# Kernel tuning notes

Measured on AMD Instinct MI355X. Metric: run time of the kernel, lower is better.

The kernel has to match this reference:

```python
import jax, jax.numpy as jnp
import numpy as np

D, H, E, K, S = 1024, 2048, 8, 2, 1  # dim, expert hidden, n_experts, top_k, n_shared
B, L = 4, 2048


def setup_inputs() -> dict:
    key = jax.random.key(0)
    ks = jax.random.split(key, 9)
    std = 0.02
    return {
        "x": jax.random.normal(ks[0], (B, L, D), dtype=jnp.float32),
        "router_w": jax.random.normal(ks[1], (E, D), dtype=jnp.float32) * std,
        "experts_bias": jnp.zeros((E,), dtype=jnp.float32),  # aux-free LB bias buffer
        "w1": jax.random.normal(ks[2], (E, D, H), dtype=jnp.float32) * std,
        "w3": jax.random.normal(ks[3], (E, D, H), dtype=jnp.float32) * std,
        "w2": jax.random.normal(ks[4], (E, H, D), dtype=jnp.float32) * std,
        "sw1": jax.random.normal(ks[5], (S, D, H), dtype=jnp.float32) * std,
        "sw3": jax.random.normal(ks[6], (S, D, H), dtype=jnp.float32) * std,
        "sw2": jax.random.normal(ks[7], (S, H, D), dtype=jnp.float32) * std,
    }


def reference(x, router_w, experts_bias, w1, w3, w2, sw1, sw3, sw2):
    b, l, d = x.shape
    xf = x.reshape(-1, d)  # [T, D], T = b*l

    # shared experts (SwiGLU FFN), summed over S
    sg = jnp.einsum("td,sdh->tsh", xf, sw1)
    su = jnp.einsum("td,sdh->tsh", xf, sw3)
    shared_out = jnp.einsum("tsh,shd->td", jax.nn.silu(sg) * su, sw2)

    # router + aux-free load-balancing bias
    logits = xf @ router_w.T + experts_bias  # [T, E]
    rw, sel = jax.lax.top_k(logits, K)       # [T, K]
    rw = jax.nn.softmax(rw.astype(jnp.float32), axis=-1).astype(x.dtype)

    # combine weights scattered to [T, E]; equals torch one_hot dispatch+index_add
    cw = (jax.nn.one_hot(sel, E, dtype=x.dtype) * rw[..., None]).sum(axis=1)

    # all-expert SwiGLU, weighted-combined (identical math: unselected weight = 0)
    g = jnp.einsum("td,edh->teh", xf, w1)
    u = jnp.einsum("td,edh->teh", xf, w3)
    eo = jax.nn.silu(g) * u  # [T, E, H]
    moe_out = jnp.einsum("te,teh,ehd->td", cw, eo, w2)

    return (moe_out + shared_out).reshape(b, l, d)
```

## Files before the change

kernel.cpp:

```cpp
#include <hip/hip_runtime.h>
#include <stdint.h>

#define T_TOK 8192
#define DIMV  1024
#define HIDV  2048
#define NE    8
#define CAP   8192
#define ROUTED 16384
#define ASSIGN_TOT 24576
#define NCAT  4096

typedef __attribute__((ext_vector_type(8))) short          bf16x8;
typedef __attribute__((ext_vector_type(8))) unsigned short u16x8;
typedef __attribute__((ext_vector_type(4))) float          floatx4;

__device__ __forceinline__ unsigned short f2bf(float f) {
    union { float f; unsigned int i; } v; v.f = f;
    unsigned int i = v.i;
    return (unsigned short)((i + 0x7FFFu + ((i >> 16) & 1u)) >> 16);
}
__device__ __forceinline__ float bf2f(unsigned short u) {
    union { unsigned int i; float f; } v; v.i = ((unsigned int)u) << 16; return v.f;
}

__device__ __forceinline__ void gll16(const void* g, void* l) {
    __builtin_amdgcn_global_load_lds((const __attribute__((address_space(1))) void*)g,
                                     (__attribute__((address_space(3))) void*)l,
                                     16, 0, 0);
}

__global__ __launch_bounds__(256) void router_kernel(
    const float* __restrict__ x,
    const float* __restrict__ rwp,
    const float* __restrict__ biasp,
    unsigned short* __restrict__ xb,
    int* __restrict__ cnt, int* __restrict__ tlist,
    int* __restrict__ pos, float* __restrict__ pw)
{
    const int t    = blockIdx.x * 4 + (threadIdx.x >> 6);
    const int lane = threadIdx.x & 63;
    const float* xr = x + (size_t)t * DIMV + lane * 16;
    float xf[16];
#pragma unroll
    for (int q = 0; q < 4; q++) {
        float4 v = *(const float4*)(xr + q * 4);
        xf[q*4+0] = v.x; xf[q*4+1] = v.y; xf[q*4+2] = v.z; xf[q*4+3] = v.w;
    }
    {
        u16x8 o0, o1;
#pragma unroll
        for (int j = 0; j < 8; j++) { o0[j] = f2bf(xf[j]); o1[j] = f2bf(xf[8 + j]); }
        unsigned short* xo = xb + (size_t)t * DIMV + lane * 16;
        *(u16x8*)xo = o0;
        *(u16x8*)(xo + 8) = o1;
    }
    float acc[NE];
#pragma unroll
    for (int e = 0; e < NE; e++) {
        const float* wr = rwp + (size_t)e * DIMV + lane * 16;
        float s = 0.f;
#pragma unroll
        for (int q = 0; q < 4; q++) {
            float4 v = *(const float4*)(wr + q * 4);
            s += xf[q*4+0]*v.x + xf[q*4+1]*v.y + xf[q*4+2]*v.z + xf[q*4+3]*v.w;
        }
        acc[e] = s;
    }
#pragma unroll
    for (int e = 0; e < NE; e++)
#pragma unroll
        for (int off = 32; off; off >>= 1) acc[e] += __shfl_xor(acc[e], off, 64);

    if (lane == 0) {
        float lg[NE];
#pragma unroll
        for (int e = 0; e < NE; e++) lg[e] = acc[e] + biasp[e];
        int e0 = 0;
#pragma unroll
        for (int e = 1; e < NE; e++) if (lg[e] > lg[e0]) e0 = e;
        int e1 = (e0 == 0) ? 1 : 0;
#pragma unroll
        for (int e = 0; e < NE; e++) if (e != e0 && lg[e] > lg[e1]) e1 = e;
        float z  = __expf(lg[e1] - lg[e0]);
        float p0 = 1.f / (1.f + z);
        float p1 = z  / (1.f + z);
        int s0 = atomicAdd(cnt + e0, 1);
        tlist[e0 * CAP + s0] = t;
        int s1 = atomicAdd(cnt + e1, 1);
        tlist[e1 * CAP + s1] = t;
        pos[2 * t + 0] = e0 * CAP + s0;
        pos[2 * t + 1] = e1 * CAP + s1;
        pw[2 * t + 0] = p0;
        pw[2 * t + 1] = p1;
    }
}

template<int R, int C>
__device__ __forceinline__ void ctrans_body(
    const float* __restrict__ src, unsigned short* __restrict__ dstp,
    unsigned short (*tile)[66], int ileave, int ubit)
{
    const int c0 = blockIdx.x * 64, r0 = blockIdx.y * 64;
    const int tid = threadIdx.x;
    const int lr = tid >> 4;
    const int lc = (tid & 15) * 4;
#pragma unroll
    for (int i = 0; i < 4; i++) {
        int r = lr + 16 * i;
        float4 v = *(const float4*)(src + (size_t)(r0 + r) * C + (c0 + lc));
        ushort4 o; o.x = f2bf(v.x); o.y = f2bf(v.y); o.z = f2bf(v.z); o.w = f2bf(v.w);
        *(ushort4*)&tile[r][lc] = o;
    }
    __syncthreads();
    const int oc  = tid >> 3;
    const int orr = (tid & 7) * 8;
#pragma unroll
    for (int i = 0; i < 2; i++) {
        int c = oc + 32 * i;
        int h = c0 + c;
        int row = ileave ? (((h >> 4) << 5) + ubit * 16 + (h & 15)) : h;
        u16x8 tmp;
#pragma unroll
        for (int j = 0; j < 8; j++) tmp[j] = tile[orr + j][c];
        *(u16x8*)(dstp + (size_t)row * R + (r0 + orr)) = tmp;
    }
}

__global__ __launch_bounds__(256) void ctrans_all(
    const float* __restrict__ w1, const float* __restrict__ w3,
    const float* __restrict__ sw1, const float* __restrict__ sw3,
    const float* __restrict__ w2, const float* __restrict__ sw2,
    unsigned short* __restrict__ wcat, unsigned short* __restrict__ scat,
    unsigned short* __restrict__ w2t, unsigned short* __restrict__ sw2t)
{
    __shared__ unsigned short tile[64][66];
    const int z = blockIdx.z;
    if (z < 18) {
        if (blockIdx.y >= DIMV / 64) return;
        const float* src; unsigned short* dstp; int u;
        if (z < 8)        { src = w1 + (size_t)z * DIMV * HIDV;       dstp = wcat + (size_t)z * NCAT * DIMV;       u = 0; }
        else if (z < 16)  { src = w3 + (size_t)(z - 8) * DIMV * HIDV; dstp = wcat + (size_t)(z - 8) * NCAT * DIMV; u = 1; }
        else if (z == 16) { src = sw1; dstp = scat; u = 0; }
        else              { src = sw3; dstp = scat; u = 1; }
        ctrans_body<DIMV, HIDV>(src, dstp, tile, 1, u);
    } else {
        if (blockIdx.x >= DIMV / 64) return;
        const float* src; unsigned short* dstp;
        if (z < 26) { src = w2 + (size_t)(z - 18) * HIDV * DIMV; dstp = w2t + (size_t)(z - 18) * DIMV * HIDV; }
        else        { src = sw2; dstp = sw2t; }
        ctrans_body<HIDV, DIMV>(src, dstp, tile, 0, 0);
    }
}


__global__ __launch_bounds__(512, 2) void up_gemm8(
    const unsigned short* __restrict__ x,
    const unsigned short* __restrict__ wcat,
    const unsigned short* __restrict__ scat,
    const int* __restrict__ cnt, const int* __restrict__ tlist,
    unsigned short* __restrict__ hbuf)
{
    const int g = blockIdx.z;
    int n_rows, row_off = 0;
    const unsigned short* Bp;
    if (g < NE) {
        for (int e = 0; e < g; e++) row_off += cnt[e];
        n_rows = cnt[g];
        Bp = wcat + (size_t)g * NCAT * DIMV;
    } else { n_rows = T_TOK; row_off = ROUTED; Bp = scat; }
    const int m0 = blockIdx.y * 256;
    if (m0 >= n_rows) return;
    const int n0 = blockIdx.x * 256;

    extern __shared__ __align__(16) unsigned short smem[];
    unsigned short* As = smem;
    unsigned short* Bs = smem + 32768;

    const int tid  = threadIdx.x;
    const int lane = tid & 63;
    const int wave = tid >> 6;
    const int wm = wave >> 2, wn = wave & 3;
    const int m16 = lane & 15, quad = lane >> 4;

    const int sr = tid >> 2;
    const int sc = (((tid & 3) ^ ((sr >> 1) & 3)) << 3);

    int tA0, tA1;
    if (g < NE) {
        int ra = m0 + sr;       if (ra >= n_rows) ra = n_rows - 1;
        int rb = m0 + 128 + sr; if (rb >= n_rows) rb = n_rows - 1;
        tA0 = tlist[g * CAP + ra];
        tA1 = tlist[g * CAP + rb];
    } else { tA0 = m0 + sr; tA1 = m0 + 128 + sr; }
    const unsigned short* sA0 = x + (size_t)tA0 * DIMV + sc;
    const unsigned short* sA1 = x + (size_t)tA1 * DIMV + sc;
    const unsigned short* sB0 = Bp + (size_t)(n0 + sr) * DIMV + sc;
    const unsigned short* sB1 = Bp + (size_t)(n0 + 128 + sr) * DIMV + sc;

    unsigned short* dA = As + wave * 512;
    unsigned short* dB = Bs + wave * 512;

#define UPSA(t, kk) { unsigned short* d_ = dA + (((t) & 1) << 14) + ((kk) << 13); \
        gll16(sA0 + (t) * 64 + (kk) * 32, d_); gll16(sA1 + (t) * 64 + (kk) * 32, d_ + 4096); }
#define UPSB(t, kk) { unsigned short* d_ = dB + (((t) & 1) << 14) + ((kk) << 13); \
        gll16(sB0 + (t) * 64 + (kk) * 32, d_); gll16(sB1 + (t) * 64 + (kk) * 32, d_ + 4096); }

    const unsigned short* Afb = As + (wm * 128 + m16) * 32 + ((quad ^ ((m16 >> 1) & 3)) << 3);
    const unsigned short* Bfb = Bs + (wn * 64  + m16) * 32 + ((quad ^ ((m16 >> 1) & 3)) << 3);

    UPSB(0, 0); UPSA(0, 0); UPSB(0, 1); UPSA(0, 1);
    UPSB(1, 0); UPSA(1, 0);
    asm volatile("s_waitcnt vmcnt(4)" ::: "memory");
    __builtin_amdgcn_s_barrier();

    floatx4 acc[8][4] = {};
    bf16x8 af[4], bfr[4];

#define NTU 16
    for (int t = 0; t < NTU; ++t) {
        const int pb = (t & 1) << 14;
        const unsigned short* Ab = Afb + pb;
        const unsigned short* Bb = Bfb + pb;
#pragma unroll
        for (int i = 0; i < 4; i++) af[i]  = *(const bf16x8*)(Ab + i * 512);
#pragma unroll
        for (int j = 0; j < 4; j++) bfr[j] = *(const bf16x8*)(Bb + j * 512);
        if (t + 1 < NTU) UPSB(t + 1, 1);
        asm volatile("s_waitcnt lgkmcnt(0)" ::: "memory");
        __builtin_amdgcn_sched_barrier(0);
        __builtin_amdgcn_s_setprio(1);
#pragma unroll
        for (int i = 0; i < 4; i++)
#pragma unroll
            for (int j = 0; j < 4; j++)
                acc[i][j] = __builtin_amdgcn_mfma_f32_16x16x32_bf16(af[i], bfr[j], acc[i][j], 0, 0, 0);
        __builtin_amdgcn_s_setprio(0);
#pragma unroll
        for (int i = 0; i < 4; i++) af[i] = *(const bf16x8*)(Ab + (4 + i) * 512);
        if (t + 1 < NTU) UPSA(t + 1, 1);
        asm volatile("s_waitcnt lgkmcnt(0)" ::: "memory");
        __builtin_amdgcn_sched_barrier(0);
        __builtin_amdgcn_s_setprio(1);
#pragma unroll
        for (int i = 0; i < 4; i++)
#pragma unroll
            for (int j = 0; j < 4; j++)
                acc[4 + i][j] = __builtin_amdgcn_mfma_f32_16x16x32_bf16(af[i], bfr[j], acc[4 + i][j], 0, 0, 0);
        __builtin_amdgcn_s_setprio(0);
        __builtin_amdgcn_s_barrier();
#pragma unroll
        for (int i = 0; i < 4; i++) af[i]  = *(const bf16x8*)(Ab + 8192 + i * 512);
#pragma unroll
        for (int j = 0; j < 4; j++) bfr[j] = *(const bf16x8*)(Bb + 8192 + j * 512);
        if (t + 2 < NTU) UPSB(t + 2, 0);
        asm volatile("s_waitcnt lgkmcnt(0)" ::: "memory");
        __builtin_amdgcn_sched_barrier(0);
        __builtin_amdgcn_s_setprio(1);
#pragma unroll
        for (int i = 0; i < 4; i++)
#pragma unroll
            for (int j = 0; j < 4; j++)
                acc[i][j] = __builtin_amdgcn_mfma_f32_16x16x32_bf16(af[i], bfr[j], acc[i][j], 0, 0, 0);
        __builtin_amdgcn_s_setprio(0);
#pragma unroll
        for (int i = 0; i < 4; i++) af[i] = *(const bf16x8*)(Ab + 8192 + (4 + i) * 512);
        if (t + 2 < NTU) UPSA(t + 2, 0);
        asm volatile("s_waitcnt lgkmcnt(0)" ::: "memory");
        __builtin_amdgcn_sched_barrier(0);
        __builtin_amdgcn_s_setprio(1);
#pragma unroll
        for (int i = 0; i < 4; i++)
#pragma unroll
            for (int j = 0; j < 4; j++)
                acc[4 + i][j] = __builtin_amdgcn_mfma_f32_16x16x32_bf16(af[i], bfr[j], acc[4 + i][j], 0, 0, 0);
        __builtin_amdgcn_s_setprio(0);
        if (t < NTU - 2) { asm volatile("s_waitcnt vmcnt(4)" ::: "memory"); }
        else             { asm volatile("s_waitcnt vmcnt(0)" ::: "memory"); }
        __builtin_amdgcn_s_barrier();
    }
#undef NTU
#undef UPSA
#undef UPSB

    const int hb = (n0 >> 1) + wn * 32;
#pragma unroll
    for (int mi = 0; mi < 8; mi++) {
#pragma unroll
        for (int ii = 0; ii < 4; ii++) {
            int r = m0 + wm * 128 + mi * 16 + quad * 4 + ii;
            if (r < n_rows) {
                unsigned short* hr = hbuf + (size_t)(row_off + r) * HIDV;
#pragma unroll
                for (int p = 0; p < 2; p++) {
                    float gv = acc[mi][2 * p][ii], uv = acc[mi][2 * p + 1][ii];
                    float s  = gv / (1.0f + __expf(-gv));
                    hr[hb + p * 16 + m16] = f2bf(s * uv);
                }
            }
        }
    }
}

__global__ __launch_bounds__(512, 2) void down_gemm8(
    const unsigned short* __restrict__ hbuf,
    const unsigned short* __restrict__ w2t,
    const unsigned short* __restrict__ sw2t,
    const int* __restrict__ cnt,
    unsigned short* __restrict__ dbuf)
{
    const int g = blockIdx.z;
    int n_rows, row_off = 0;
    const unsigned short* Bp;
    if (g < NE) {
        for (int e = 0; e < g; e++) row_off += cnt[e];
        n_rows = cnt[g];
        Bp = w2t + (size_t)g * DIMV * HIDV;
    } else { n_rows = T_TOK; row_off = ROUTED; Bp = sw2t; }
    const int m0 = blockIdx.y * 256;
    if (m0 >= n_rows) return;
    const int n0 = blockIdx.x * 256;

    extern __shared__ __align__(16) unsigned short smem[];
    unsigned short* As = smem;
    unsigned short* Bs = smem + 32768;

    const int tid  = threadIdx.x;
    const int lane = tid & 63;
    const int wave = tid >> 6;
    const int wm = wave >> 2, wn = wave & 3;
    const int m16 = lane & 15, quad = lane >> 4;

    const int sr = tid >> 2;
    const int sc = (((tid & 3) ^ ((sr >> 1) & 3)) << 3);

    const unsigned short* sA0 = hbuf + (size_t)(row_off + m0 + sr) * HIDV + sc;
    const unsigned short* sA1 = sA0 + (size_t)128 * HIDV;
    const unsigned short* sB0 = Bp + (size_t)(n0 + sr) * HIDV + sc;
    const unsigned short* sB1 = sB0 + (size_t)128 * HIDV;

    unsigned short* dA = As + wave * 512;
    unsigned short* dB = Bs + wave * 512;

#define DNSA(t, kk) { unsigned short* d_ = dA + (((t) & 1) << 14) + ((kk) << 13); \
        gll16(sA0 + (t) * 64 + (kk) * 32, d_); gll16(sA1 + (t) * 64 + (kk) * 32, d_ + 4096); }
#define DNSB(t, kk) { unsigned short* d_ = dB + (((t) & 1) << 14) + ((kk) << 13); \
        gll16(sB0 + (t) * 64 + (kk) * 32, d_); gll16(sB1 + (t) * 64 + (kk) * 32, d_ + 4096); }

    const unsigned short* Afb = As + (wm * 128 + m16) * 32 + ((quad ^ ((m16 >> 1) & 3)) << 3);
    const unsigned short* Bfb = Bs + (wn * 64  + m16) * 32 + ((quad ^ ((m16 >> 1) & 3)) << 3);

    DNSB(0, 0); DNSA(0, 0); DNSB(0, 1); DNSA(0, 1);
    DNSB(1, 0); DNSA(1, 0);
    asm volatile("s_waitcnt vmcnt(4)" ::: "memory");
    __builtin_amdgcn_s_barrier();

    floatx4 acc[8][4] = {};
    bf16x8 af[4], bfr[4];

#define NTD 32
    for (int t = 0; t < NTD; ++t) {
        const int pb = (t & 1) << 14;
        const unsigned short* Ab = Afb + pb;
        const unsigned short* Bb = Bfb + pb;
#pragma unroll
        for (int i = 0; i < 4; i++) af[i]  = *(const bf16x8*)(Ab + i * 512);
#pragma unroll
        for (int j = 0; j < 4; j++) bfr[j] = *(const bf16x8*)(Bb + j * 512);
        if (t + 1 < NTD) DNSB(t + 1, 1);
        asm volatile("s_waitcnt lgkmcnt(0)" ::: "memory");
        __builtin_amdgcn_sched_barrier(0);
        __builtin_amdgcn_s_setprio(1);
#pragma unroll
        for (int i = 0; i < 4; i++)
#pragma unroll
            for (int j = 0; j < 4; j++)
                acc[i][j] = __builtin_amdgcn_mfma_f32_16x16x32_bf16(af[i], bfr[j], acc[i][j], 0, 0, 0);
        __builtin_amdgcn_s_setprio(0);
#pragma unroll
        for (int i = 0; i < 4; i++) af[i] = *(const bf16x8*)(Ab + (4 + i) * 512);
        if (t + 1 < NTD) DNSA(t + 1, 1);
        asm volatile("s_waitcnt lgkmcnt(0)" ::: "memory");
        __builtin_amdgcn_sched_barrier(0);
        __builtin_amdgcn_s_setprio(1);
#pragma unroll
        for (int i = 0; i < 4; i++)
#pragma unroll
            for (int j = 0; j < 4; j++)
                acc[4 + i][j] = __builtin_amdgcn_mfma_f32_16x16x32_bf16(af[i], bfr[j], acc[4 + i][j], 0, 0, 0);
        __builtin_amdgcn_s_setprio(0);
        __builtin_amdgcn_s_barrier();
#pragma unroll
        for (int i = 0; i < 4; i++) af[i]  = *(const bf16x8*)(Ab + 8192 + i * 512);
#pragma unroll
        for (int j = 0; j < 4; j++) bfr[j] = *(const bf16x8*)(Bb + 8192 + j * 512);
        if (t + 2 < NTD) DNSB(t + 2, 0);
        asm volatile("s_waitcnt lgkmcnt(0)" ::: "memory");
        __builtin_amdgcn_sched_barrier(0);
        __builtin_amdgcn_s_setprio(1);
#pragma unroll
        for (int i = 0; i < 4; i++)
#pragma unroll
            for (int j = 0; j < 4; j++)
                acc[i][j] = __builtin_amdgcn_mfma_f32_16x16x32_bf16(af[i], bfr[j], acc[i][j], 0, 0, 0);
        __builtin_amdgcn_s_setprio(0);
#pragma unroll
        for (int i = 0; i < 4; i++) af[i] = *(const bf16x8*)(Ab + 8192 + (4 + i) * 512);
        if (t + 2 < NTD) DNSA(t + 2, 0);
        asm volatile("s_waitcnt lgkmcnt(0)" ::: "memory");
        __builtin_amdgcn_sched_barrier(0);
        __builtin_amdgcn_s_setprio(1);
#pragma unroll
        for (int i = 0; i < 4; i++)
#pragma unroll
            for (int j = 0; j < 4; j++)
                acc[4 + i][j] = __builtin_amdgcn_mfma_f32_16x16x32_bf16(af[i], bfr[j], acc[4 + i][j], 0, 0, 0);
        __builtin_amdgcn_s_setprio(0);
        if (t < NTD - 2) { asm volatile("s_waitcnt vmcnt(4)" ::: "memory"); }
        else             { asm volatile("s_waitcnt vmcnt(0)" ::: "memory"); }
        __builtin_amdgcn_s_barrier();
    }
#undef NTD
#undef DNSA
#undef DNSB

#pragma unroll
    for (int mi = 0; mi < 8; mi++) {
#pragma unroll
        for (int ii = 0; ii < 4; ii++) {
            int r = m0 + wm * 128 + mi * 16 + quad * 4 + ii;
            if (r < n_rows) {
                unsigned short* drow = dbuf + (size_t)(row_off + r) * DIMV;
#pragma unroll
                for (int nj = 0; nj < 4; nj++)
                    drow[n0 + wn * 64 + nj * 16 + m16] = f2bf(acc[mi][nj][ii]);
            }
        }
    }
}

__global__ __launch_bounds__(256) void combine_kernel(
    const unsigned short* __restrict__ dbuf,
    const int* __restrict__ cnt, const int* __restrict__ pos,
    const float* __restrict__ pw, float* __restrict__ outp)
{
    const int tid = threadIdx.x;
    const int t = blockIdx.x * 2 + (tid >> 7);
    const int c = (tid & 127) * 8;
    int goff[NE];
    {
        int s = 0;
#pragma unroll
        for (int e = 0; e < NE; e++) { goff[e] = s; s += cnt[e]; }
    }
    const int p0 = pos[2 * t], p1 = pos[2 * t + 1];
    const float w0 = pw[2 * t], w1 = pw[2 * t + 1];
    const int r0 = goff[p0 >> 13] + (p0 & (CAP - 1));
    const int r1 = goff[p1 >> 13] + (p1 & (CAP - 1));
    const u16x8 v0 = *(const u16x8*)(dbuf + (size_t)r0 * DIMV + c);
    const u16x8 v1 = *(const u16x8*)(dbuf + (size_t)r1 * DIMV + c);
    const u16x8 vs = *(const u16x8*)(dbuf + (size_t)(ROUTED + t) * DIMV + c);
    float o[8];
#pragma unroll
    for (int j = 0; j < 8; j++)
        o[j] = w0 * bf2f(v0[j]) + w1 * bf2f(v1[j]) + bf2f(vs[j]);
    float* op = outp + (size_t)t * DIMV + c;
    *(float4*)op       = make_float4(o[0], o[1], o[2], o[3]);
    *(float4*)(op + 4) = make_float4(o[4], o[5], o[6], o[7]);
}

extern "C" void kernel_launch(void* const* d_in, const int* in_sizes, int n_in,
                              void* d_out, int out_size, void* d_ws, size_t ws_size,
                              hipStream_t stream)
{
    (void)in_sizes; (void)n_in; (void)out_size; (void)ws_size;
    const float* x    = (const float*)d_in[0];
    const float* rw   = (const float*)d_in[1];
    const float* bias = (const float*)d_in[2];
    const float* w1   = (const float*)d_in[3];
    const float* w3   = (const float*)d_in[4];
    const float* w2   = (const float*)d_in[5];
    const float* sw1  = (const float*)d_in[6];
    const float* sw3  = (const float*)d_in[7];
    const float* sw2  = (const float*)d_in[8];
    float* outp = (float*)d_out;

    char* p = (char*)d_ws;
    auto alloc = [&](size_t b) { char* r = p; p += (b + 255) & ~(size_t)255; return r; };
    int*   cnt   = (int*)  alloc(64);
    int*   tlist = (int*)  alloc((size_t)NE * CAP * 4);
    int*   pos   = (int*)  alloc((size_t)T_TOK * 2 * 4);
    float* pw    = (float*)alloc((size_t)T_TOK * 2 * 4);
    unsigned short* xb   = (unsigned short*)alloc((size_t)T_TOK * DIMV * 2);
    unsigned short* hbuf = (unsigned short*)alloc((size_t)ASSIGN_TOT * HIDV * 2);
    unsigned short* wcat = (unsigned short*)alloc((size_t)NE * NCAT * DIMV * 2);
    unsigned short* scat = (unsigned short*)alloc((size_t)NCAT * DIMV * 2);
    unsigned short* w2t  = (unsigned short*)alloc((size_t)NE * DIMV * HIDV * 2);
    unsigned short* sw2t = (unsigned short*)alloc((size_t)DIMV * HIDV * 2);
    unsigned short* dbuf = wcat;

    hipMemsetAsync(cnt, 0, 64, stream);

    dim3 blk(256);
    router_kernel<<<dim3(T_TOK/4), blk, 0, stream>>>(x, rw, bias, xb, cnt, tlist, pos, pw);
    ctrans_all<<<dim3(HIDV/64, HIDV/64, 27), blk, 0, stream>>>(w1, w3, sw1, sw3, w2, sw2,
                                                               wcat, scat, w2t, sw2t);
    up_gemm8<<<dim3(NCAT/256, 32, 9), dim3(512), 131072, stream>>>(xb, wcat, scat,
                                                                   cnt, tlist, hbuf);
    down_gemm8<<<dim3(DIMV/256, 32, 9), dim3(512), 131072, stream>>>(hbuf, w2t, sw2t,
                                                                     cnt, dbuf);
    combine_kernel<<<dim3(T_TOK/2), blk, 0, stream>>>(dbuf, cnt, pos, pw, outp);
}
```

Measured before the change: 791.6 us.

## Switch expert GEMMs to 32x32x16 MFMA with remapped tiles and swizzled block order

Both the up and down grouped GEMMs now use 32x32x16 bf16 MFMA instructions instead of 16x16x32. This halves the LDS fragment reads per MFMA and drops the explicit lgkmcnt waits and sched barriers inside the loop. The gate/up interleave in the weight transpose changes from 16-row to 32-row groups to match the new accumulator layout, and the epilogues are rewritten for the 32x32 output layout. Block indices are also remapped so that blocks launched consecutively spread across N tiles, which is meant to improve L2 reuse. The risk is that the compiler now schedules LDS waits itself, which could hurt overlap of loads with MFMA work.

```diff
diff --git a/kernel.cpp b/kernel.cpp
--- a/kernel.cpp
+++ b/kernel.cpp
@@ -10,9 +10,10 @@
 #define ASSIGN_TOT 24576
 #define NCAT  4096
 
-typedef __attribute__((ext_vector_type(8))) short          bf16x8;
-typedef __attribute__((ext_vector_type(8))) unsigned short u16x8;
-typedef __attribute__((ext_vector_type(4))) float          floatx4;
+typedef __attribute__((ext_vector_type(8)))  short          bf16x8;
+typedef __attribute__((ext_vector_type(8)))  unsigned short u16x8;
+typedef __attribute__((ext_vector_type(4)))  float          floatx4;
+typedef __attribute__((ext_vector_type(16))) float          floatx16;
 
 __device__ __forceinline__ unsigned short f2bf(float f) {
     union { float f; unsigned int i; } v; v.f = f;
@@ -118,7 +119,7 @@
     for (int i = 0; i < 2; i++) {
         int c = oc + 32 * i;
         int h = c0 + c;
-        int row = ileave ? (((h >> 4) << 5) + ubit * 16 + (h & 15)) : h;
+        int row = ileave ? (((h >> 5) << 6) + (ubit << 5) + (h & 31)) : h;
         u16x8 tmp;
 #pragma unroll
         for (int j = 0; j < 8; j++) tmp[j] = tile[orr + j][c];
@@ -168,9 +169,12 @@
         n_rows = cnt[g];
         Bp = wcat + (size_t)g * NCAT * DIMV;
     } else { n_rows = T_TOK; row_off = ROUTED; Bp = scat; }
-    const int m0 = blockIdx.y * 256;
+
+    const int p_lin = blockIdx.y * 16 + blockIdx.x;
+    const int work  = (p_lin & 7) * 64 + (p_lin >> 3);
+    const int n0 = (work >> 5) * 256;
+    const int m0 = (work & 31) * 256;
     if (m0 >= n_rows) return;
-    const int n0 = blockIdx.x * 256;
 
     extern __shared__ __align__(16) unsigned short smem[];
     unsigned short* As = smem;
@@ -180,7 +184,12 @@
     const int lane = tid & 63;
     const int wave = tid >> 6;
     const int wm = wave >> 2, wn = wave & 3;
-    const int m16 = lane & 15, quad = lane >> 4;
+    const int r5 = lane & 31, hi = lane >> 5;
+    const int sw3 = (r5 >> 1) & 3;
+    const int c0c = hi ^ (sw3 & 1);
+    const int s1  = (sw3 >> 1) & 1;
+    const int k0o = s1 << 4;
+    const int k1o = (1 ^ s1) << 4;
 
     const int sr = tid >> 2;
     const int sc = (((tid & 3) ^ ((sr >> 1) & 3)) << 3);
@@ -205,74 +214,73 @@
 #define UPSB(t, kk) { unsigned short* d_ = dB + (((t) & 1) << 14) + ((kk) << 13); \
         gll16(sB0 + (t) * 64 + (kk) * 32, d_); gll16(sB1 + (t) * 64 + (kk) * 32, d_ + 4096); }
 
-    const unsigned short* Afb = As + (wm * 128 + m16) * 32 + ((quad ^ ((m16 >> 1) & 3)) << 3);
-    const unsigned short* Bfb = Bs + (wn * 64  + m16) * 32 + ((quad ^ ((m16 >> 1) & 3)) << 3);
+    const int aob = (wm * 128 + r5) * 32 + c0c * 8;
+    const int bob = (wn * 64  + r5) * 32 + c0c * 8;
 
     UPSB(0, 0); UPSA(0, 0); UPSB(0, 1); UPSA(0, 1);
+    asm volatile("" ::: "memory");
     UPSB(1, 0); UPSA(1, 0);
     asm volatile("s_waitcnt vmcnt(4)" ::: "memory");
     __builtin_amdgcn_s_barrier();
 
-    floatx4 acc[8][4] = {};
-    bf16x8 af[4], bfr[4];
+    floatx16 acc[4][2] = {};
+    bf16x8 af[4], bfr[2];
 
 #define NTU 16
     for (int t = 0; t < NTU; ++t) {
         const int pb = (t & 1) << 14;
-        const unsigned short* Ab = Afb + pb;
-        const unsigned short* Bb = Bfb + pb;
-#pragma unroll
-        for (int i = 0; i < 4; i++) af[i]  = *(const bf16x8*)(Ab + i * 512);
-#pragma unroll
-        for (int j = 0; j < 4; j++) bfr[j] = *(const bf16x8*)(Bb + j * 512);
-        if (t + 1 < NTU) UPSB(t + 1, 1);
-        asm volatile("s_waitcnt lgkmcnt(0)" ::: "memory");
-        __builtin_amdgcn_sched_barrier(0);
         __builtin_amdgcn_s_setprio(1);
-#pragma unroll
-        for (int i = 0; i < 4; i++)
-#pragma unroll
-            for (int j = 0; j < 4; j++)
-                acc[i][j] = __builtin_amdgcn_mfma_f32_16x16x32_bf16(af[i], bfr[j], acc[i][j], 0, 0, 0);
-        __builtin_amdgcn_s_setprio(0);
-#pragma unroll
-        for (int i = 0; i < 4; i++) af[i] = *(const bf16x8*)(Ab + (4 + i) * 512);
-        if (t + 1 < NTU) UPSA(t + 1, 1);
-        asm volatile("s_waitcnt lgkmcnt(0)" ::: "memory");
-        __builtin_amdgcn_sched_barrier(0);
-        __builtin_amdgcn_s_setprio(1);
-#pragma unroll
-        for (int i = 0; i < 4; i++)
-#pragma unroll
-            for (int j = 0; j < 4; j++)
-                acc[4 + i][j] = __builtin_amdgcn_mfma_f32_16x16x32_bf16(af[i], bfr[j], acc[4 + i][j], 0, 0, 0);
+        {
+            const unsigned short* Ab = As + aob + pb;
+            const unsigned short* Bb = Bs + bob + pb;
+#pragma unroll
+            for (int i = 0; i < 4; i++) af[i]  = *(const bf16x8*)(Ab + k0o + i * 1024);
+#pragma unroll
+            for (int j = 0; j < 2; j++) bfr[j] = *(const bf16x8*)(Bb + k0o + j * 1024);
+            if (t + 1 < NTU) UPSB(t + 1, 1);
+#pragma unroll
+            for (int i = 0; i < 4; i++)
+#pragma unroll
+                for (int j = 0; j < 2; j++)
+                    acc[i][j] = __builtin_amdgcn_mfma_f32_32x32x16_bf16(af[i], bfr[j], acc[i][j], 0, 0, 0);
+#pragma unroll
+            for (int i = 0; i < 4; i++) af[i]  = *(const bf16x8*)(Ab + k1o + i * 1024);
+#pragma unroll
+            for (int j = 0; j < 2; j++) bfr[j] = *(const bf16x8*)(Bb + k1o + j * 1024);
+            if (t + 1 < NTU) UPSA(t + 1, 1);
+#pragma unroll
+            for (int i = 0; i < 4; i++)
+#pragma unroll
+                for (int j = 0; j < 2; j++)
+                    acc[i][j] = __builtin_amdgcn_mfma_f32_32x32x16_bf16(af[i], bfr[j], acc[i][j], 0, 0, 0);
+        }
         __builtin_amdgcn_s_setprio(0);
         __builtin_amdgcn_s_barrier();
-#pragma unroll
-        for (int i = 0; i < 4; i++) af[i]  = *(const bf16x8*)(Ab + 8192 + i * 512);
-#pragma unroll
-        for (int j = 0; j < 4; j++) bfr[j] = *(const bf16x8*)(Bb + 8192 + j * 512);
-        if (t + 2 < NTU) UPSB(t + 2, 0);
-        asm volatile("s_waitcnt lgkmcnt(0)" ::: "memory");
-        __builtin_amdgcn_sched_barrier(0);
         __builtin_amdgcn_s_setprio(1);
-#pragma unroll
-        for (int i = 0; i < 4; i++)
-#pragma unroll
-            for (int j = 0; j < 4; j++)
-                acc[i][j] = __builtin_amdgcn_mfma_f32_16x16x32_bf16(af[i], bfr[j], acc[i][j], 0, 0, 0);
-        __builtin_amdgcn_s_setprio(0);
-#pragma unroll
-        for (int i = 0; i < 4; i++) af[i] = *(const bf16x8*)(Ab + 8192 + (4 + i) * 512);
-        if (t + 2 < NTU) UPSA(t + 2, 0);
-        asm volatile("s_waitcnt lgkmcnt(0)" ::: "memory");
-        __builtin_amdgcn_sched_barrier(0);
-        __builtin_amdgcn_s_setprio(1);
-#pragma unroll
-        for (int i = 0; i < 4; i++)
-#pragma unroll
-            for (int j = 0; j < 4; j++)
-                acc[4 + i][j] = __builtin_amdgcn_mfma_f32_16x16x32_bf16(af[i], bfr[j], acc[4 + i][j], 0, 0, 0);
+        {
+            const unsigned short* Ab = As + aob + pb + 8192;
+            const unsigned short* Bb = Bs + bob + pb + 8192;
+#pragma unroll
+            for (int i = 0; i < 4; i++) af[i]  = *(const bf16x8*)(Ab + k0o + i * 1024);
+#pragma unroll
+            for (int j = 0; j < 2; j++) bfr[j] = *(const bf16x8*)(Bb + k0o + j * 1024);
+            if (t + 2 < NTU) UPSB(t + 2, 0);
+#pragma unroll
+            for (int i = 0; i < 4; i++)
+#pragma unroll
+                for (int j = 0; j < 2; j++)
+                    acc[i][j] = __builtin_amdgcn_mfma_f32_32x32x16_bf16(af[i], bfr[j], acc[i][j], 0, 0, 0);
+#pragma unroll
+            for (int i = 0; i < 4; i++) af[i]  = *(const bf16x8*)(Ab + k1o + i * 1024);
+#pragma unroll
+            for (int j = 0; j < 2; j++) bfr[j] = *(const bf16x8*)(Bb + k1o + j * 1024);
+            if (t + 2 < NTU) UPSA(t + 2, 0);
+#pragma unroll
+            for (int i = 0; i < 4; i++)
+#pragma unroll
+                for (int j = 0; j < 2; j++)
+                    acc[i][j] = __builtin_amdgcn_mfma_f32_32x32x16_bf16(af[i], bfr[j], acc[i][j], 0, 0, 0);
+        }
         __builtin_amdgcn_s_setprio(0);
         if (t < NTU - 2) { asm volatile("s_waitcnt vmcnt(4)" ::: "memory"); }
         else             { asm volatile("s_waitcnt vmcnt(0)" ::: "memory"); }
@@ -282,20 +290,16 @@
 #undef UPSA
 #undef UPSB
 
-    const int hb = (n0 >> 1) + wn * 32;
-#pragma unroll
-    for (int mi = 0; mi < 8; mi++) {
-#pragma unroll
-        for (int ii = 0; ii < 4; ii++) {
-            int r = m0 + wm * 128 + mi * 16 + quad * 4 + ii;
-            if (r < n_rows) {
-                unsigned short* hr = hbuf + (size_t)(row_off + r) * HIDV;
-#pragma unroll
-                for (int p = 0; p < 2; p++) {
-                    float gv = acc[mi][2 * p][ii], uv = acc[mi][2 * p + 1][ii];
-                    float s  = gv / (1.0f + __expf(-gv));
-                    hr[hb + p * 16 + m16] = f2bf(s * uv);
-                }
+    const int hb = (n0 + wn * 64) >> 1;
+#pragma unroll
+    for (int mi = 0; mi < 4; mi++) {
+#pragma unroll
+        for (int r = 0; r < 16; r++) {
+            int row = m0 + wm * 128 + mi * 32 + (r & 3) + 8 * (r >> 2) + 4 * hi;
+            if (row < n_rows) {
+                float gv = acc[mi][0][r], uv = acc[mi][1][r];
+                float s  = gv / (1.0f + __expf(-gv));
+                hbuf[(size_t)(row_off + row) * HIDV + hb + r5] = f2bf(s * uv);
             }
         }
     }
@@ -316,9 +320,12 @@
         n_rows = cnt[g];
         Bp = w2t + (size_t)g * DIMV * HIDV;
     } else { n_rows = T_TOK; row_off = ROUTED; Bp = sw2t; }
-    const int m0 = blockIdx.y * 256;
+
+    const int p_lin = blockIdx.y * 4 + blockIdx.x;
+    const int work  = (p_lin & 7) * 16 + (p_lin >> 3);
+    const int n0 = (work >> 5) * 256;
+    const int m0 = (work & 31) * 256;
     if (m0 >= n_rows) return;
-    const int n0 = blockIdx.x * 256;
 
     extern __shared__ __align__(16) unsigned short smem[];
     unsigned short* As = smem;
@@ -328,7 +335,12 @@
     const int lane = tid & 63;
     const int wave = tid >> 6;
     const int wm = wave >> 2, wn = wave & 3;
-    const int m16 = lane & 15, quad = lane >> 4;
+    const int r5 = lane & 31, hi = lane >> 5;
+    const int sw3 = (r5 >> 1) & 3;
+    const int c0c = hi ^ (sw3 & 1);
+    const int s1  = (sw3 >> 1) & 1;
+    const int k0o = s1 << 4;
+    const int k1o = (1 ^ s1) << 4;
 
     const int sr = tid >> 2;
     const int sc = (((tid & 3) ^ ((sr >> 1) & 3)) << 3);
@@ -346,74 +358,73 @@
 #define DNSB(t, kk) { unsigned short* d_ = dB + (((t) & 1) << 14) + ((kk) << 13); \
         gll16(sB0 + (t) * 64 + (kk) * 32, d_); gll16(sB1 + (t) * 64 + (kk) * 32, d_ + 4096); }
 
-    const unsigned short* Afb = As + (wm * 128 + m16) * 32 + ((quad ^ ((m16 >> 1) & 3)) << 3);
-    const unsigned short* Bfb = Bs + (wn * 64  + m16) * 32 + ((quad ^ ((m16 >> 1) & 3)) << 3);
+    const int aob = (wm * 128 + r5) * 32 + c0c * 8;
+    const int bob = (wn * 64  + r5) * 32 + c0c * 8;
 
     DNSB(0, 0); DNSA(0, 0); DNSB(0, 1); DNSA(0, 1);
+    asm volatile("" ::: "memory");
     DNSB(1, 0); DNSA(1, 0);
     asm volatile("s_waitcnt vmcnt(4)" ::: "memory");
     __builtin_amdgcn_s_barrier();
 
-    floatx4 acc[8][4] = {};
-    bf16x8 af[4], bfr[4];
+    floatx16 acc[4][2] = {};
+    bf16x8 af[4], bfr[2];
 
 #define NTD 32
     for (int t = 0; t < NTD; ++t) {
         const int pb = (t & 1) << 14;
-        const unsigned short* Ab = Afb + pb;
-        const unsigned short* Bb = Bfb + pb;
-#pragma unroll
-        for (int i = 0; i < 4; i++) af[i]  = *(const bf16x8*)(Ab + i * 512);
-#pragma unroll
-        for (int j = 0; j < 4; j++) bfr[j] = *(const bf16x8*)(Bb + j * 512);
-        if (t + 1 < NTD) DNSB(t + 1, 1);
-        asm volatile("s_waitcnt lgkmcnt(0)" ::: "memory");
-        __builtin_amdgcn_sched_barrier(0);
         __builtin_amdgcn_s_setprio(1);
-#pragma unroll
-        for (int i = 0; i < 4; i++)
-#pragma unroll
-            for (int j = 0; j < 4; j++)
-                acc[i][j] = __builtin_amdgcn_mfma_f32_16x16x32_bf16(af[i], bfr[j], acc[i][j], 0, 0, 0);
-        __builtin_amdgcn_s_setprio(0);
-#pragma unroll
-        for (int i = 0; i < 4; i++) af[i] = *(const bf16x8*)(Ab + (4 + i) * 512);
-        if (t + 1 < NTD) DNSA(t + 1, 1);
-        asm volatile("s_waitcnt lgkmcnt(0)" ::: "memory");
-        __builtin_amdgcn_sched_barrier(0);
-        __builtin_amdgcn_s_setprio(1);
-#pragma unroll
-        for (int i = 0; i < 4; i++)
-#pragma unroll
-            for (int j = 0; j < 4; j++)
-                acc[4 + i][j] = __builtin_amdgcn_mfma_f32_16x16x32_bf16(af[i], bfr[j], acc[4 + i][j], 0, 0, 0);
+        {
+            const unsigned short* Ab = As + aob + pb;
+            const unsigned short* Bb = Bs + bob + pb;
+#pragma unroll
+            for (int i = 0; i < 4; i++) af[i]  = *(const bf16x8*)(Ab + k0o + i * 1024);
+#pragma unroll
+            for (int j = 0; j < 2; j++) bfr[j] = *(const bf16x8*)(Bb + k0o + j * 1024);
+            if (t + 1 < NTD) DNSB(t + 1, 1);
+#pragma unroll
+            for (int i = 0; i < 4; i++)
+#pragma unroll
+                for (int j = 0; j < 2; j++)
+                    acc[i][j] = __builtin_amdgcn_mfma_f32_32x32x16_bf16(af[i], bfr[j], acc[i][j], 0, 0, 0);
+#pragma unroll
+            for (int i = 0; i < 4; i++) af[i]  = *(const bf16x8*)(Ab + k1o + i * 1024);
+#pragma unroll
+            for (int j = 0; j < 2; j++) bfr[j] = *(const bf16x8*)(Bb + k1o + j * 1024);
+            if (t + 1 < NTD) DNSA(t + 1, 1);
+#pragma unroll
+            for (int i = 0; i < 4; i++)
+#pragma unroll
+                for (int j = 0; j < 2; j++)
+                    acc[i][j] = __builtin_amdgcn_mfma_f32_32x32x16_bf16(af[i], bfr[j], acc[i][j], 0, 0, 0);
+        }
         __builtin_amdgcn_s_setprio(0);
         __builtin_amdgcn_s_barrier();
-#pragma unroll
-        for (int i = 0; i < 4; i++) af[i]  = *(const bf16x8*)(Ab + 8192 + i * 512);
-#pragma unroll
-        for (int j = 0; j < 4; j++) bfr[j] = *(const bf16x8*)(Bb + 8192 + j * 512);
-        if (t + 2 < NTD) DNSB(t + 2, 0);
-        asm volatile("s_waitcnt lgkmcnt(0)" ::: "memory");
-        __builtin_amdgcn_sched_barrier(0);
         __builtin_amdgcn_s_setprio(1);
-#pragma unroll
-        for (int i = 0; i < 4; i++)
-#pragma unroll
-            for (int j = 0; j < 4; j++)
-                acc[i][j] = __builtin_amdgcn_mfma_f32_16x16x32_bf16(af[i], bfr[j], acc[i][j], 0, 0, 0);
-        __builtin_amdgcn_s_setprio(0);
-#pragma unroll
-        for (int i = 0; i < 4; i++) af[i] = *(const bf16x8*)(Ab + 8192 + (4 + i) * 512);
-        if (t + 2 < NTD) DNSA(t + 2, 0);
-        asm volatile("s_waitcnt lgkmcnt(0)" ::: "memory");
-        __builtin_amdgcn_sched_barrier(0);
-        __builtin_amdgcn_s_setprio(1);
-#pragma unroll
-        for (int i = 0; i < 4; i++)
-#pragma unroll
-            for (int j = 0; j < 4; j++)
-                acc[4 + i][j] = __builtin_amdgcn_mfma_f32_16x16x32_bf16(af[i], bfr[j], acc[4 + i][j], 0, 0, 0);
+        {
+            const unsigned short* Ab = As + aob + pb + 8192;
+            const unsigned short* Bb = Bs + bob + pb + 8192;
+#pragma unroll
+            for (int i = 0; i < 4; i++) af[i]  = *(const bf16x8*)(Ab + k0o + i * 1024);
+#pragma unroll
+            for (int j = 0; j < 2; j++) bfr[j] = *(const bf16x8*)(Bb + k0o + j * 1024);
+            if (t + 2 < NTD) DNSB(t + 2, 0);
+#pragma unroll
+            for (int i = 0; i < 4; i++)
+#pragma unroll
+                for (int j = 0; j < 2; j++)
+                    acc[i][j] = __builtin_amdgcn_mfma_f32_32x32x16_bf16(af[i], bfr[j], acc[i][j], 0, 0, 0);
+#pragma unroll
+            for (int i = 0; i < 4; i++) af[i]  = *(const bf16x8*)(Ab + k1o + i * 1024);
+#pragma unroll
+            for (int j = 0; j < 2; j++) bfr[j] = *(const bf16x8*)(Bb + k1o + j * 1024);
+            if (t + 2 < NTD) DNSA(t + 2, 0);
+#pragma unroll
+            for (int i = 0; i < 4; i++)
+#pragma unroll
+                for (int j = 0; j < 2; j++)
+                    acc[i][j] = __builtin_amdgcn_mfma_f32_32x32x16_bf16(af[i], bfr[j], acc[i][j], 0, 0, 0);
+        }
         __builtin_amdgcn_s_setprio(0);
         if (t < NTD - 2) { asm volatile("s_waitcnt vmcnt(4)" ::: "memory"); }
         else             { asm volatile("s_waitcnt vmcnt(0)" ::: "memory"); }
@@ -424,15 +435,16 @@
 #undef DNSB
 
 #pragma unroll
-    for (int mi = 0; mi < 8; mi++) {
-#pragma unroll
-        for (int ii = 0; ii < 4; ii++) {
-            int r = m0 + wm * 128 + mi * 16 + quad * 4 + ii;
-            if (r < n_rows) {
-                unsigned short* drow = dbuf + (size_t)(row_off + r) * DIMV;
-#pragma unroll
-                for (int nj = 0; nj < 4; nj++)
-                    drow[n0 + wn * 64 + nj * 16 + m16] = f2bf(acc[mi][nj][ii]);
+    for (int mi = 0; mi < 4; mi++) {
+#pragma unroll
+        for (int nj = 0; nj < 2; nj++) {
+#pragma unroll
+            for (int r = 0; r < 16; r++) {
+                int row = m0 + wm * 128 + mi * 32 + (r & 3) + 8 * (r >> 2) + 4 * hi;
+                if (row < n_rows) {
+                    int col = n0 + wn * 64 + nj * 32 + r5;
+                    dbuf[(size_t)(row_off + row) * DIMV + col] = f2bf(acc[mi][nj][r]);
+                }
             }
         }
     }
@@ -504,9 +516,9 @@
     router_kernel<<<dim3(T_TOK/4), blk, 0, stream>>>(x, rw, bias, xb, cnt, tlist, pos, pw);
     ctrans_all<<<dim3(HIDV/64, HIDV/64, 27), blk, 0, stream>>>(w1, w3, sw1, sw3, w2, sw2,
                                                                wcat, scat, w2t, sw2t);
-    up_gemm8<<<dim3(NCAT/256, 32, 9), dim3(512), 131072, stream>>>(xb, wcat, scat,
-                                                                   cnt, tlist, hbuf);
-    down_gemm8<<<dim3(DIMV/256, 32, 9), dim3(512), 131072, stream>>>(hbuf, w2t, sw2t,
-                                                                     cnt, dbuf);
+    up_gemm8<<<dim3(16, 32, 9), dim3(512), 131072, stream>>>(xb, wcat, scat,
+                                                             cnt, tlist, hbuf);
+    down_gemm8<<<dim3(4, 32, 9), dim3(512), 131072, stream>>>(hbuf, w2t, sw2t,
+                                                              cnt, dbuf);
     combine_kernel<<<dim3(T_TOK/2), blk, 0, stream>>>(dbuf, cnt, pos, pw, outp);
 }
```

Result: slower. 859.2 us (+8.5%).
